# Kernel optimization log

Measured on AMD Instinct MI355X. Metric: run time of the kernel, lower is better.

## Reference

```python
import jax, jax.numpy as jnp
import numpy as np

DIM = 1280
N_HEADS = 10
HEAD_DIM = 128
BASE = 10000.0
BATCH = 2
SEQ = 2048


def _rope(x):
    # x: [b, h, s, d]; matches source: split even/odd channels, rotate, concat halves
    b, h, s, d = x.shape
    theta = 1.0 / (BASE ** (jnp.arange(0, d, 2, dtype=jnp.float32) / d))  # [d/2]
    ang = jnp.arange(s, dtype=jnp.float32)[:, None] * theta               # [s, d/2]
    cos = jnp.cos(ang)
    sin = jnp.sin(ang)
    x1 = x[..., 0::2]
    x2 = x[..., 1::2]
    return jnp.concatenate([x1 * cos - x2 * sin, x1 * sin + x2 * cos], axis=-1)


def setup_inputs() -> dict:
    key = jax.random.key(0)
    ks = jax.random.split(key, 6)
    w_std = 0.02
    x = jax.random.normal(ks[0], (BATCH, SEQ, DIM), dtype=jnp.float32)
    positions = jnp.arange(SEQ, dtype=jnp.int64 if jax.config.jax_enable_x64 else jnp.int32)
    Wq = jax.random.normal(ks[1], (DIM, DIM), dtype=jnp.float32) * w_std
    Wk = jax.random.normal(ks[2], (DIM, DIM), dtype=jnp.float32) * w_std
    Wv = jax.random.normal(ks[3], (DIM, DIM), dtype=jnp.float32) * w_std
    Wo = jax.random.normal(ks[4], (DIM, DIM), dtype=jnp.float32) * w_std
    bq = jnp.zeros((DIM,), jnp.float32)
    bk = jnp.zeros((DIM,), jnp.float32)
    bv = jnp.zeros((DIM,), jnp.float32)
    bo = jnp.zeros((DIM,), jnp.float32)
    return {"x": x, "positions": positions, "Wq": Wq, "bq": bq, "Wk": Wk,
            "bk": bk, "Wv": Wv, "bv": bv, "Wo": Wo, "bo": bo}


def reference(x, positions, Wq, bq, Wk, bk, Wv, bv, Wo, bo):
    b, s, _ = x.shape
    scale = 1.0 / np.sqrt(HEAD_DIM)

    def proj(W, bias):
        y = jnp.einsum('bsd,ed->bse', x, W) + bias  # Linear: x @ W^T + b
        return y.reshape(b, s, N_HEADS, HEAD_DIM).transpose(0, 2, 1, 3)

    q = _rope(proj(Wq, bq))  # [b, h, s, hd]
    k = _rope(proj(Wk, bk))
    v = proj(Wv, bv)

    scores = jnp.einsum('bhqd,bhkd->bhqk', q, k) * scale
    causal = jnp.tril(jnp.ones((s, s), dtype=bool))
    scores = jnp.where(causal, scores, jnp.float32(-jnp.inf))
    attn = jax.nn.softmax(scores, axis=-1)
    out = jnp.einsum('bhqk,bhkd->bhqd', attn, v)
    out = out.transpose(0, 2, 1, 3).reshape(b, s, N_HEADS * HEAD_DIM)
    return jnp.einsum('bse,de->bsd', out, Wo) + bo
```

## Files before the change

### kernel.cpp

```cpp
#include <hip/hip_runtime.h>
#include <cmath>

typedef unsigned short u16;
typedef __attribute__((ext_vector_type(8))) short bf16x8;
typedef __attribute__((ext_vector_type(4))) float f32x4;

#define B_    2
#define SEQ_  2048
#define NH_   10
#define HD_   128
#define DIM_  1280

__device__ __forceinline__ u16 f2bf(float f) {
    union { float f; unsigned u; } v; v.f = f;
    unsigned r = (v.u + 0x7fffu + ((v.u >> 16) & 1u)) >> 16;
    return (u16)r;
}
__device__ __forceinline__ float bf2f(u16 h) {
    union { unsigned u; float f; } v; v.u = ((unsigned)h) << 16;
    return v.f;
}
__device__ __forceinline__ f32x4 mfma16(bf16x8 a, bf16x8 b, f32x4 c) {
    return __builtin_amdgcn_mfma_f32_16x16x32_bf16(a, b, c, 0, 0, 0);
}
__device__ __forceinline__ void g2l16(const void* g, void* l) {
    __builtin_amdgcn_global_load_lds(
        (const __attribute__((address_space(1))) unsigned*)g,
        (__attribute__((address_space(3))) unsigned*)l, 16, 0, 0);
}

__global__ void sincos_tab(float* __restrict__ ct, float* __restrict__ st) {
    int idx = blockIdx.x * 256 + threadIdx.x;
    int s = idx >> 6, j = idx & 63;
    float e = (float)j * (1.0f / 64.0f);
    float theta = 1.0f / powf(10000.0f, e);
    float ang = (float)s * theta;
    ct[idx] = cosf(ang);
    st[idx] = sinf(ang);
}

__global__ __launch_bounds__(256) void cvt_k(const float* __restrict__ x,
                                             const float* __restrict__ w0,
                                             const float* __restrict__ w1,
                                             const float* __restrict__ w2,
                                             const float* __restrict__ w3,
                                             u16* __restrict__ xb,
                                             u16* __restrict__ d0,
                                             u16* __restrict__ d1,
                                             u16* __restrict__ d2,
                                             u16* __restrict__ d3) {
    const int NX = B_ * SEQ_ * DIM_;
    const int WN = DIM_ * DIM_;
    int i = (blockIdx.x * 256 + threadIdx.x) * 8;
    const float* src; u16* dst; int off;
    if (i < NX) { src = x; dst = xb; off = i; }
    else {
        int j = i - NX; int w = j / WN; off = j - w * WN;
        src = (w == 0) ? w0 : (w == 1) ? w1 : (w == 2) ? w2 : w3;
        dst = (w == 0) ? d0 : (w == 1) ? d1 : (w == 2) ? d2 : d3;
    }
    float4 a0 = *(const float4*)(src + off);
    float4 a1 = *(const float4*)(src + off + 4);
    union { uint4 q; u16 u[8]; } t;
    t.u[0] = f2bf(a0.x); t.u[1] = f2bf(a0.y);
    t.u[2] = f2bf(a0.z); t.u[3] = f2bf(a0.w);
    t.u[4] = f2bf(a1.x); t.u[5] = f2bf(a1.y);
    t.u[6] = f2bf(a1.z); t.u[7] = f2bf(a1.w);
    *(uint4*)(dst + off) = t.q;
}

template <typename OT>
__device__ __forceinline__ void gemm_core(const u16* __restrict__ A,
                                          const u16* __restrict__ W,
                                          const float* __restrict__ bias,
                                          OT* __restrict__ C,
                                          int m_blk, int n_blk,
                                          u16* As, u16* Bs) {
    const int tid = threadIdx.x;
    const int wave = tid >> 6, lane = tid & 63;
    const int quad = lane >> 4, l16 = lane & 15;
    const int w_m = (wave >> 1) * 64, w_n = (wave & 1) * 64;
    const int srow = wave * 32;
    const int lrow = lane >> 2;
    const int csw = ((lane & 3) ^ ((lane >> 3) & 3)) * 8;
    const int rsw = (l16 >> 1) & 3;
    f32x4 acc[4][4] = {};

    const u16* pa = A + (size_t)(m_blk + srow + lrow) * DIM_ + csw;
    const u16* pb = W + (size_t)(n_blk + srow + lrow) * DIM_ + csw;
    u16* la0 = As + srow * 32;
    u16* la1 = As + (srow + 16) * 32;
    u16* lb0 = Bs + srow * 32;
    u16* lb1 = Bs + (srow + 16) * 32;

    for (int k0 = 0; k0 < DIM_; k0 += 32) {
        g2l16(pa + k0, la0);
        g2l16(pa + k0 + 16 * DIM_, la1);
        g2l16(pb + k0, lb0);
        g2l16(pb + k0 + 16 * DIM_, lb1);
        __syncthreads();
        bf16x8 af[4], bf[4];
        #pragma unroll
        for (int mt = 0; mt < 4; ++mt)
            af[mt] = *(const bf16x8*)&As[(w_m + mt * 16 + l16) * 32
                                         + (quad ^ rsw) * 8];
        #pragma unroll
        for (int nt = 0; nt < 4; ++nt)
            bf[nt] = *(const bf16x8*)&Bs[(w_n + nt * 16 + l16) * 32
                                         + (quad ^ rsw) * 8];
        #pragma unroll
        for (int mt = 0; mt < 4; ++mt)
            #pragma unroll
            for (int nt = 0; nt < 4; ++nt)
                acc[mt][nt] = mfma16(af[mt], bf[nt], acc[mt][nt]);
        __syncthreads();
    }
    #pragma unroll
    for (int nt = 0; nt < 4; ++nt) {
        int col = n_blk + w_n + nt * 16 + l16;
        float bv = bias[col];
        #pragma unroll
        for (int mt = 0; mt < 4; ++mt) {
            #pragma unroll
            for (int r = 0; r < 4; ++r) {
                int row = m_blk + w_m + mt * 16 + quad * 4 + r;
                float v = acc[mt][nt][r] + bv;
                if constexpr (sizeof(OT) == 4) C[(size_t)row * DIM_ + col] = v;
                else C[(size_t)row * DIM_ + col] = (OT)f2bf(v);
            }
        }
    }
}

__global__ __launch_bounds__(256) void qkv_gemm(const u16* __restrict__ xb,
                                                const u16* __restrict__ Wqb,
                                                const u16* __restrict__ Wkb,
                                                const u16* __restrict__ Wvb,
                                                const float* __restrict__ bq,
                                                const float* __restrict__ bk,
                                                const float* __restrict__ bv,
                                                u16* __restrict__ Qb,
                                                u16* __restrict__ Kb,
                                                u16* __restrict__ Vb) {
    __shared__ alignas(16) u16 As[128 * 32];
    __shared__ alignas(16) u16 Bs[128 * 32];
    int bx = blockIdx.x;
    int wsel = bx / 10, n_blk = (bx % 10) * 128, m_blk = blockIdx.y * 128;
    const u16* W = (wsel == 0) ? Wqb : (wsel == 1) ? Wkb : Wvb;
    const float* bias = (wsel == 0) ? bq : (wsel == 1) ? bk : bv;
    u16* C = (wsel == 0) ? Qb : (wsel == 1) ? Kb : Vb;
    gemm_core<u16>(xb, W, bias, C, m_blk, n_blk, As, Bs);
}

__global__ __launch_bounds__(256) void out_gemm(const u16* __restrict__ AO,
                                                const u16* __restrict__ Wob,
                                                const float* __restrict__ bo,
                                                float* __restrict__ C) {
    __shared__ alignas(16) u16 As[128 * 32];
    __shared__ alignas(16) u16 Bs[128 * 32];
    gemm_core<float>(AO, Wob, bo, C, blockIdx.y * 128, blockIdx.x * 128, As, Bs);
}

__global__ __launch_bounds__(256) void rope_k(const u16* __restrict__ Qs_,
                                              const u16* __restrict__ Ks_,
                                              u16* __restrict__ Qd,
                                              u16* __restrict__ Kp,
                                              const float* __restrict__ ct,
                                              const float* __restrict__ st,
                                              float qscale) {
    int t = blockIdx.x * 256 + threadIdx.x;
    const int NR = B_ * SEQ_ * NH_;
    int rid = t >> 3, j0 = (t & 7) * 8;
    const bool isQ = (rid < NR);
    const u16* src = isQ ? Qs_ : Ks_;
    float sc = isQ ? qscale : 1.0f;
    if (!isQ) rid -= NR;
    int h = rid % NH_;
    int s = (rid / NH_) % SEQ_;
    int b = rid / (NH_ * SEQ_);
    const u16* p = src + (size_t)rid * HD_ + 2 * j0;
    union { uint4 q; u16 u[8]; } a0, a1, o1, o2;
    a0.q = *(const uint4*)p;
    a1.q = *(const uint4*)(p + 8);
    const float* cc = ct + (size_t)s * 64 + j0;
    const float* ss = st + (size_t)s * 64 + j0;
    #pragma unroll
    for (int j = 0; j < 8; ++j) {
        float x1 = bf2f((j < 4) ? a0.u[2 * j] : a1.u[2 * j - 8]);
        float x2 = bf2f((j < 4) ? a0.u[2 * j + 1] : a1.u[2 * j - 7]);
        float c = cc[j], sn = ss[j];
        o1.u[j] = f2bf((x1 * c - x2 * sn) * sc);
        o2.u[j] = f2bf((x1 * sn + x2 * c) * sc);
    }
    if (isQ) {
        u16* q = Qd + (size_t)(((size_t)b * SEQ_ + s) * NH_ + h) * HD_;
        *(uint4*)(q + j0) = o1.q;
        *(uint4*)(q + 64 + j0) = o2.q;
    } else {
        int kt = s >> 6, key = s & 63, nt = key >> 4, l16k = key & 15;
        int qd = (j0 >> 3) & 3;
        int kk1 = j0 >> 5, kk2 = 2 + kk1;
        u16* tb = Kp + ((size_t)((b * NH_ + h) * 32 + kt)) * 8192;
        int lane = qd * 16 + l16k;
        *(uint4*)(tb + (kk1 * 4 + nt) * 512 + lane * 8) = o1.q;
        *(uint4*)(tb + (kk2 * 4 + nt) * 512 + lane * 8) = o2.q;
    }
}

__global__ __launch_bounds__(256) void transpose_v(const u16* __restrict__ V,
                                                   u16* __restrict__ Vp) {
    __shared__ u16 T[128][72];
    int stile = blockIdx.x, h = blockIdx.y, b = blockIdx.z;
    int tid = threadIdx.x;
    {
        int sl = tid >> 2, d0 = (tid & 3) * 32;
        const u16* vp = V + ((size_t)((b * SEQ_ + stile * 64 + sl) * NH_ + h)) * HD_ + d0;
        #pragma unroll
        for (int i = 0; i < 4; ++i) {
            union { uint4 q; u16 u[8]; } r;
            r.q = *(const uint4*)(vp + i * 8);
            #pragma unroll
            for (int j = 0; j < 8; ++j) T[d0 + i * 8 + j][sl] = r.u[j];
        }
    }
    __syncthreads();
    {
        int d = tid >> 1, kc = (tid & 1) * 32;
        int dt = d >> 4, l16v = d & 15, kk = kc >> 5;
        u16* tb = Vp + ((size_t)((b * NH_ + h) * 32 + stile)) * 8192 + (kk * 8 + dt) * 512;
        #pragma unroll
        for (int i = 0; i < 4; ++i)
            *(uint4*)(tb + (i * 16 + l16v) * 8) = *(const uint4*)&T[d][kc + i * 8];
    }
}

__device__ const unsigned char QT_TAB[40] =
    {0,1,2,3,4,4,5,5,6,6,7,7,8,8,8,9,9,9,10,10,10,11,11,11,
     12,12,12,12,13,13,13,13,14,14,14,14,15,15,15,15};
__device__ const unsigned char CH_TAB[40] =
    {0,0,0,0,0,1,0,1,0,1,0,1,0,1,2,0,1,2,0,1,2,0,1,2,
     0,1,2,3,0,1,2,3,0,1,2,3,0,1,2,3};

__global__ __launch_bounds__(256, 3) void attn_k(const u16* __restrict__ Q,
                                                 const u16* __restrict__ Kp,
                                                 const u16* __restrict__ Vp,
                                                 u16* __restrict__ AO,
                                                 u16* __restrict__ PO,
                                                 float* __restrict__ Pm,
                                                 float* __restrict__ Pl) {
    const int cid = blockIdx.x, h = blockIdx.y, b = blockIdx.z;
    const int qt = QT_TAB[cid], c = CH_TAB[cid];
    const int ntiles = 2 * qt + 2;
    const int nch = (ntiles + 7) >> 3;
    const int kt0 = c * 8;
    const int kt1 = (kt0 + 8 < ntiles) ? kt0 + 8 : ntiles;
    const int bh = b * NH_ + h;

    const int tid = threadIdx.x, wave = tid >> 6, lane = tid & 63;
    const int quad = lane >> 4, l16 = lane & 15;

    __shared__ alignas(16) u16 Ks[16 * 512];
    __shared__ alignas(16) u16 Vs[16 * 512];
    __shared__ alignas(16) u16 Pt[4][4][512];

    bf16x8 qf[2][4];
    #pragma unroll
    for (int mt = 0; mt < 2; ++mt) {
        int sq = qt * 128 + wave * 32 + mt * 16 + l16;
        const u16* qp = Q + ((size_t)((b * SEQ_ + sq) * NH_ + h)) * HD_;
        #pragma unroll
        for (int kk = 0; kk < 4; ++kk)
            qf[mt][kk] = *(const bf16x8*)(qp + kk * 32 + quad * 8);
    }
    f32x4 oacc[2][8] = {};
    float m_run[2] = {-INFINITY, -INFINITY};
    float l_run[2] = {0.f, 0.f};
    const int q0 = qt * 128 + wave * 32 + l16;

    const u16* kpb = Kp + ((size_t)bh * 32) * 8192;
    const u16* vpb = Vp + ((size_t)bh * 32) * 8192;

    for (int kt = kt0; kt < kt1; ++kt) {
        const u16* kp_t = kpb + (size_t)kt * 8192;
        const u16* vp_t = vpb + (size_t)kt * 8192;
        #pragma unroll
        for (int i = 0; i < 4; ++i) {
            int f = wave * 4 + i;
            g2l16(kp_t + f * 512 + lane * 8, &Ks[f * 512]);
            g2l16(vp_t + f * 512 + lane * 8, &Vs[f * 512]);
        }
        __syncthreads();
        f32x4 sacc[2][4] = {};
        #pragma unroll
        for (int kk = 0; kk < 4; ++kk) {
            #pragma unroll
            for (int nt = 0; nt < 4; ++nt) {
                bf16x8 kf = *(const bf16x8*)&Ks[(kk * 4 + nt) * 512 + lane * 8];
                sacc[0][nt] = mfma16(kf, qf[0][kk], sacc[0][nt]);
                sacc[1][nt] = mfma16(kf, qf[1][kk], sacc[1][nt]);
            }
        }
        const bool maskt = (kt >= 2 * qt);
        const int keyb = kt * 64 + quad * 4;
        #pragma unroll
        for (int mt = 0; mt < 2; ++mt) {
            const int qg = q0 + mt * 16;
            float sv[16];
            #pragma unroll
            for (int nt = 0; nt < 4; ++nt)
                #pragma unroll
                for (int r = 0; r < 4; ++r) {
                    float x = sacc[mt][nt][r];
                    if (maskt && (keyb + nt * 16 + r > qg)) x = -INFINITY;
                    sv[nt * 4 + r] = x;
                }
            float tm = sv[0];
            #pragma unroll
            for (int i = 1; i < 16; ++i) tm = fmaxf(tm, sv[i]);
            tm = fmaxf(tm, __shfl_xor(tm, 16, 64));
            tm = fmaxf(tm, __shfl_xor(tm, 32, 64));
            float mn = fmaxf(m_run[mt], tm);
            float al = __builtin_amdgcn_exp2f(m_run[mt] - mn);
            float ps = 0.f;
            #pragma unroll
            for (int nt = 0; nt < 4; ++nt) {
                float p0 = __builtin_amdgcn_exp2f(sv[nt * 4 + 0] - mn);
                float p1 = __builtin_amdgcn_exp2f(sv[nt * 4 + 1] - mn);
                float p2 = __builtin_amdgcn_exp2f(sv[nt * 4 + 2] - mn);
                float p3 = __builtin_amdgcn_exp2f(sv[nt * 4 + 3] - mn);
                ps += p0 + p1 + p2 + p3;
                ushort4 w4;
                w4.x = f2bf(p0); w4.y = f2bf(p1); w4.z = f2bf(p2); w4.w = f2bf(p3);
                int rowf = (((nt & 1) << 1) | (quad >> 1)) * 16 + l16;
                *(ushort4*)&Pt[wave][mt * 2 + (nt >> 1)][rowf * 8 + (quad & 1) * 4] = w4;
            }
            ps += __shfl_xor(ps, 16, 64);
            ps += __shfl_xor(ps, 32, 64);
            l_run[mt] = l_run[mt] * al + ps;
            m_run[mt] = mn;
            #pragma unroll
            for (int dt = 0; dt < 8; ++dt)
                #pragma unroll
                for (int r = 0; r < 4; ++r) oacc[mt][dt][r] *= al;
        }
        #pragma unroll
        for (int kk = 0; kk < 2; ++kk) {
            bf16x8 pf0 = *(const bf16x8*)&Pt[wave][kk][(quad * 16 + l16) * 8];
            bf16x8 pf1 = *(const bf16x8*)&Pt[wave][2 + kk][(quad * 16 + l16) * 8];
            #pragma unroll
            for (int dt = 0; dt < 8; ++dt) {
                bf16x8 vf = *(const bf16x8*)&Vs[(kk * 8 + dt) * 512 + lane * 8];
                oacc[0][dt] = mfma16(vf, pf0, oacc[0][dt]);
                oacc[1][dt] = mfma16(vf, pf1, oacc[1][dt]);
            }
        }
        __syncthreads();
    }
    if (nch == 1) {
        #pragma unroll
        for (int mt = 0; mt < 2; ++mt) {
            float invl = 1.0f / l_run[mt];
            int sq = q0 + mt * 16;
            u16* op = AO + ((size_t)((b * SEQ_ + sq) * NH_ + h)) * HD_ + quad * 4;
            #pragma unroll
            for (int dt = 0; dt < 8; ++dt) {
                ushort4 w4;
                w4.x = f2bf(oacc[mt][dt][0] * invl);
                w4.y = f2bf(oacc[mt][dt][1] * invl);
                w4.z = f2bf(oacc[mt][dt][2] * invl);
                w4.w = f2bf(oacc[mt][dt][3] * invl);
                *(ushort4*)(op + dt * 16) = w4;
            }
        }
    } else {
        size_t pidx = ((size_t)bh * 16 + qt) * 4 + c;
        u16* po = PO + pidx * 16384;
        #pragma unroll
        for (int mt = 0; mt < 2; ++mt) {
            #pragma unroll
            for (int dt = 0; dt < 8; ++dt) {
                ushort4 w4;
                w4.x = f2bf(oacc[mt][dt][0]);
                w4.y = f2bf(oacc[mt][dt][1]);
                w4.z = f2bf(oacc[mt][dt][2]);
                w4.w = f2bf(oacc[mt][dt][3]);
                *(ushort4*)(po + ((wave * 16 + mt * 8 + dt) * 64 + lane) * 4) = w4;
            }
            if (quad == 0) {
                Pm[pidx * 128 + wave * 32 + mt * 16 + l16] = m_run[mt];
                Pl[pidx * 128 + wave * 32 + mt * 16 + l16] = l_run[mt];
            }
        }
    }
}

__global__ __launch_bounds__(256) void combine_k(const u16* __restrict__ PO,
                                                 const float* __restrict__ Pm,
                                                 const float* __restrict__ Pl,
                                                 u16* __restrict__ AO) {
    const int qt = 4 + blockIdx.x, h = blockIdx.y, b = blockIdx.z;
    const int nch = (2 * qt + 2 + 7) >> 3;
    const int bh = b * NH_ + h;
    const int tid = threadIdx.x;
    const int q = tid >> 1, dh = tid & 1;
    const int wave = q >> 5, mt = (q >> 4) & 1, l16 = q & 15;
    size_t base = ((size_t)bh * 16 + qt) * 4;

    float mv[4], wgt[4];
    float M = -INFINITY;
    for (int c = 0; c < nch; ++c) {
        mv[c] = Pm[(base + c) * 128 + q];
        M = fmaxf(M, mv[c]);
    }
    float L = 0.f;
    for (int c = 0; c < nch; ++c) {
        wgt[c] = __builtin_amdgcn_exp2f(mv[c] - M);
        L += wgt[c] * Pl[(base + c) * 128 + q];
    }
    float o[64];
    #pragma unroll
    for (int j = 0; j < 64; ++j) o[j] = 0.f;
    for (int c = 0; c < nch; ++c) {
        const u16* p = PO + (base + c) * 16384;
        float wc = wgt[c];
        #pragma unroll
        for (int dtl = 0; dtl < 4; ++dtl) {
            int dt = dh * 4 + dtl;
            #pragma unroll
            for (int quad = 0; quad < 4; ++quad) {
                union { ushort4 v; u16 u[4]; } t;
                t.v = *(const ushort4*)(p + ((wave * 16 + mt * 8 + dt) * 64
                                             + quad * 16 + l16) * 4);
                #pragma unroll
                for (int r = 0; r < 4; ++r)
                    o[dtl * 16 + quad * 4 + r] += wc * bf2f(t.u[r]);
            }
        }
    }
    float invL = 1.0f / L;
    int sq = qt * 128 + q;
    u16* op = AO + ((size_t)((b * SEQ_ + sq) * NH_ + h)) * HD_ + dh * 64;
    union { uint4 v[8]; u16 u[64]; } t;
    #pragma unroll
    for (int j = 0; j < 64; ++j) t.u[j] = f2bf(o[j] * invL);
    #pragma unroll
    for (int i = 0; i < 8; ++i) *(uint4*)(op + i * 8) = t.v[i];
}

extern "C" void kernel_launch(void* const* d_in, const int* in_sizes, int n_in,
                              void* d_out, int out_size, void* d_ws, size_t ws_size,
                              hipStream_t stream) {
    const float* x  = (const float*)d_in[0];
    const float* Wq = (const float*)d_in[2];
    const float* bq = (const float*)d_in[3];
    const float* Wk = (const float*)d_in[4];
    const float* bk = (const float*)d_in[5];
    const float* Wv = (const float*)d_in[6];
    const float* bv = (const float*)d_in[7];
    const float* Wo = (const float*)d_in[8];
    const float* bo = (const float*)d_in[9];
    float* out = (float*)d_out;

    const size_t NE = (size_t)B_ * SEQ_ * NH_ * HD_;
    const size_t WN = (size_t)DIM_ * DIM_;
    u16* Qb  = (u16*)d_ws;
    u16* Kb  = Qb + NE;
    u16* Vb  = Kb + NE;
    u16* Vp  = Vb + NE;
    u16* xb  = Vp + NE;
    u16* Wqb = xb + NE;
    u16* Wkb = Wqb + WN;
    u16* Wvb = Wkb + WN;
    u16* Wob = Wvb + WN;
    float* ct = (float*)(Wob + WN);
    float* st = ct + (size_t)SEQ_ * 64;
    u16* PO  = (u16*)(st + (size_t)SEQ_ * 64);
    float* Pm = (float*)(PO + (size_t)B_ * NH_ * 16 * 4 * 16384);
    float* Pl = Pm + (size_t)B_ * NH_ * 16 * 4 * 128;
    u16* Qr = Vb;
    u16* Kp = xb;
    u16* AO = Qb;

    sincos_tab<<<(SEQ_ * 64) / 256, 256, 0, stream>>>(ct, st);

    const int NCVT = (B_ * SEQ_ * DIM_ + 4 * (int)WN) / 8 / 256;
    cvt_k<<<NCVT, 256, 0, stream>>>(x, Wq, Wk, Wv, Wo, xb, Wqb, Wkb, Wvb, Wob);

    qkv_gemm<<<dim3(30, 32), 256, 0, stream>>>(xb, Wqb, Wkb, Wvb, bq, bk, bv,
                                               Qb, Kb, Vb);

    transpose_v<<<dim3(SEQ_ / 64, NH_, B_), 256, 0, stream>>>(Vb, Vp);

    const float qsc = 0.08838834764831845f * 1.4426950408889634f;
    rope_k<<<(2 * B_ * SEQ_ * NH_ * 8) / 256, 256, 0, stream>>>(Qb, Kb, Qr, Kp,
                                                                ct, st, qsc);

    attn_k<<<dim3(40, NH_, B_), 256, 0, stream>>>(Qr, Kp, Vp, AO, PO, Pm, Pl);
    combine_k<<<dim3(12, NH_, B_), 256, 0, stream>>>(PO, Pm, Pl, AO);

    out_gemm<<<dim3(10, 32), 256, 0, stream>>>(AO, Wob, bo, out);
}
```

Measured before the change: 287.5 us.

## Prefetch GEMM tiles through registers and fold sincos table into convert kernel

The shared GEMM core no longer loads tiles directly from global memory into LDS and then waits on them. It now prefetches the next K-slice into registers while the current slice is being multiplied, then stores it to LDS at the top of the next iteration, so global latency overlaps with MFMA work. The sincos table is computed by extra blocks appended to the convert kernel, which removes one kernel launch. The register prefetch raises register pressure and adds explicit LDS stores, and a small pack4 helper tidies the bf16 packing.

```diff
diff --git a/kernel.cpp b/kernel.cpp
--- a/kernel.cpp
+++ b/kernel.cpp
@@ -28,15 +28,9 @@
         (const __attribute__((address_space(1))) unsigned*)g,
         (__attribute__((address_space(3))) unsigned*)l, 16, 0, 0);
 }
-
-__global__ void sincos_tab(float* __restrict__ ct, float* __restrict__ st) {
-    int idx = blockIdx.x * 256 + threadIdx.x;
-    int s = idx >> 6, j = idx & 63;
-    float e = (float)j * (1.0f / 64.0f);
-    float theta = 1.0f / powf(10000.0f, e);
-    float ang = (float)s * theta;
-    ct[idx] = cosf(ang);
-    st[idx] = sinf(ang);
+__device__ __forceinline__ ushort4 pack4(float a, float b, float c, float d) {
+    ushort4 w; w.x = f2bf(a); w.y = f2bf(b); w.z = f2bf(c); w.w = f2bf(d);
+    return w;
 }
 
 __global__ __launch_bounds__(256) void cvt_k(const float* __restrict__ x,
@@ -48,10 +42,24 @@
                                              u16* __restrict__ d0,
                                              u16* __restrict__ d1,
                                              u16* __restrict__ d2,
-                                             u16* __restrict__ d3) {
+                                             u16* __restrict__ d3,
+                                             float* __restrict__ ct,
+                                             float* __restrict__ st) {
     const int NX = B_ * SEQ_ * DIM_;
     const int WN = DIM_ * DIM_;
-    int i = (blockIdx.x * 256 + threadIdx.x) * 8;
+    const int NCV = (NX + 4 * WN) / 8 / 256;
+    int bid = blockIdx.x;
+    if (bid >= NCV) {
+        int idx = (bid - NCV) * 256 + threadIdx.x;
+        int s = idx >> 6, j = idx & 63;
+        float e = (float)j * (1.0f / 64.0f);
+        float theta = 1.0f / powf(10000.0f, e);
+        float ang = (float)s * theta;
+        ct[idx] = cosf(ang);
+        st[idx] = sinf(ang);
+        return;
+    }
+    int i = (bid * 256 + threadIdx.x) * 8;
     const float* src; u16* dst; int off;
     if (i < NX) { src = x; dst = xb; off = i; }
     else {
@@ -88,17 +96,29 @@
 
     const u16* pa = A + (size_t)(m_blk + srow + lrow) * DIM_ + csw;
     const u16* pb = W + (size_t)(n_blk + srow + lrow) * DIM_ + csw;
-    u16* la0 = As + srow * 32;
-    u16* la1 = As + (srow + 16) * 32;
-    u16* lb0 = Bs + srow * 32;
-    u16* lb1 = Bs + (srow + 16) * 32;
+    u16* la0 = As + (srow + lrow) * 32 + (lane & 3) * 8;
+    u16* la1 = la0 + 16 * 32;
+    u16* lb0 = Bs + (srow + lrow) * 32 + (lane & 3) * 8;
+    u16* lb1 = lb0 + 16 * 32;
+
+    uint4 ra0 = *(const uint4*)(pa);
+    uint4 ra1 = *(const uint4*)(pa + 16 * DIM_);
+    uint4 rb0 = *(const uint4*)(pb);
+    uint4 rb1 = *(const uint4*)(pb + 16 * DIM_);
 
     for (int k0 = 0; k0 < DIM_; k0 += 32) {
-        g2l16(pa + k0, la0);
-        g2l16(pa + k0 + 16 * DIM_, la1);
-        g2l16(pb + k0, lb0);
-        g2l16(pb + k0 + 16 * DIM_, lb1);
         __syncthreads();
+        *(uint4*)la0 = ra0;
+        *(uint4*)la1 = ra1;
+        *(uint4*)lb0 = rb0;
+        *(uint4*)lb1 = rb1;
+        __syncthreads();
+        if (k0 + 32 < DIM_) {
+            ra0 = *(const uint4*)(pa + k0 + 32);
+            ra1 = *(const uint4*)(pa + k0 + 32 + 16 * DIM_);
+            rb0 = *(const uint4*)(pb + k0 + 32);
+            rb1 = *(const uint4*)(pb + k0 + 32 + 16 * DIM_);
+        }
         bf16x8 af[4], bf[4];
         #pragma unroll
         for (int mt = 0; mt < 4; ++mt)
@@ -113,7 +133,6 @@
             #pragma unroll
             for (int nt = 0; nt < 4; ++nt)
                 acc[mt][nt] = mfma16(af[mt], bf[nt], acc[mt][nt]);
-        __syncthreads();
     }
     #pragma unroll
     for (int nt = 0; nt < 4; ++nt) {
@@ -329,8 +348,7 @@
                 float p2 = __builtin_amdgcn_exp2f(sv[nt * 4 + 2] - mn);
                 float p3 = __builtin_amdgcn_exp2f(sv[nt * 4 + 3] - mn);
                 ps += p0 + p1 + p2 + p3;
-                ushort4 w4;
-                w4.x = f2bf(p0); w4.y = f2bf(p1); w4.z = f2bf(p2); w4.w = f2bf(p3);
+                ushort4 w4 = pack4(p0, p1, p2, p3);
                 int rowf = (((nt & 1) << 1) | (quad >> 1)) * 16 + l16;
                 *(ushort4*)&Pt[wave][mt * 2 + (nt >> 1)][rowf * 8 + (quad & 1) * 4] = w4;
             }
@@ -364,11 +382,8 @@
             u16* op = AO + ((size_t)((b * SEQ_ + sq) * NH_ + h)) * HD_ + quad * 4;
             #pragma unroll
             for (int dt = 0; dt < 8; ++dt) {
-                ushort4 w4;
-                w4.x = f2bf(oacc[mt][dt][0] * invl);
-                w4.y = f2bf(oacc[mt][dt][1] * invl);
-                w4.z = f2bf(oacc[mt][dt][2] * invl);
-                w4.w = f2bf(oacc[mt][dt][3] * invl);
+                ushort4 w4 = pack4(oacc[mt][dt][0] * invl, oacc[mt][dt][1] * invl,
+                                   oacc[mt][dt][2] * invl, oacc[mt][dt][3] * invl);
                 *(ushort4*)(op + dt * 16) = w4;
             }
         }
@@ -379,11 +394,8 @@
         for (int mt = 0; mt < 2; ++mt) {
             #pragma unroll
             for (int dt = 0; dt < 8; ++dt) {
-                ushort4 w4;
-                w4.x = f2bf(oacc[mt][dt][0]);
-                w4.y = f2bf(oacc[mt][dt][1]);
-                w4.z = f2bf(oacc[mt][dt][2]);
-                w4.w = f2bf(oacc[mt][dt][3]);
+                ushort4 w4 = pack4(oacc[mt][dt][0], oacc[mt][dt][1],
+                                   oacc[mt][dt][2], oacc[mt][dt][3]);
                 *(ushort4*)(po + ((wave * 16 + mt * 8 + dt) * 64 + lane) * 4) = w4;
             }
             if (quad == 0) {
@@ -481,10 +493,9 @@
     u16* Kp = xb;
     u16* AO = Qb;
 
-    sincos_tab<<<(SEQ_ * 64) / 256, 256, 0, stream>>>(ct, st);
-
     const int NCVT = (B_ * SEQ_ * DIM_ + 4 * (int)WN) / 8 / 256;
-    cvt_k<<<NCVT, 256, 0, stream>>>(x, Wq, Wk, Wv, Wo, xb, Wqb, Wkb, Wvb, Wob);
+    cvt_k<<<NCVT + 512, 256, 0, stream>>>(x, Wq, Wk, Wv, Wo,
+                                          xb, Wqb, Wkb, Wvb, Wob, ct, st);
 
     qkv_gemm<<<dim3(30, 32), 256, 0, stream>>>(xb, Wqb, Wkb, Wvb, bq, bk, bv,
                                                Qb, Kb, Vb);
```

Measured after the change: 286.4 us. Within noise of the previous version (-0.4%).
